# Kernel optimization log

Measured on AMD Instinct MI355X. Metric: run time of the kernel, lower is better.

The kernel has to match this reference:

```python
import jax, jax.numpy as jnp
import numpy as np

N_SEQ = 100_000
N_LAB = 64
E_CON = 1_600_000
D_IN = 128; D_HID = 128; BEL_OUT = 64; INC_OUT = 128
BN_EPS = 1e-5


def setup_inputs() -> dict:
    key = jax.random.key(0)
    ks = jax.random.split(key, 16)
    def W(k, i, o):
        return jax.random.normal(k, (i, o), jnp.float32) / np.float32(np.sqrt(i))
    return {
        "x_seq": jax.random.normal(ks[0], (N_SEQ, D_IN), jnp.float32),
        "x_label": jax.random.normal(ks[1], (N_LAB, D_IN), jnp.float32),
        "W1_bel": W(ks[2], D_IN, D_HID), "b1_bel": jnp.zeros((D_HID,), jnp.float32),
        "W1_inc": W(ks[3], D_IN, D_HID), "b1_inc": jnp.zeros((D_HID,), jnp.float32),
        "W1_con": W(ks[4], D_IN, D_HID), "b1_con": jnp.zeros((D_HID,), jnp.float32),
        "g1s": jnp.ones((D_HID,), jnp.float32), "beta1s": jnp.zeros((D_HID,), jnp.float32),
        "g1l": jnp.ones((D_HID,), jnp.float32), "beta1l": jnp.zeros((D_HID,), jnp.float32),
        "W2_bel": W(ks[5], D_HID, BEL_OUT), "b2_bel": jnp.zeros((BEL_OUT,), jnp.float32),
        "W2_inc": W(ks[6], D_HID, INC_OUT), "b2_inc": jnp.zeros((INC_OUT,), jnp.float32),
        "W2_con": W(ks[7], D_HID, INC_OUT), "b2_con": jnp.zeros((INC_OUT,), jnp.float32),
        "g2s": jnp.ones((INC_OUT,), jnp.float32), "beta2s": jnp.zeros((INC_OUT,), jnp.float32),
        "g2l": jnp.ones((BEL_OUT,), jnp.float32), "beta2l": jnp.zeros((BEL_OUT,), jnp.float32),
        "bel_label": jax.random.randint(ks[8], (N_SEQ,), 0, N_LAB),
        "con_src": jax.random.randint(ks[9], (E_CON,), 0, N_SEQ),
        "con_dst": jax.random.randint(ks[10], (E_CON,), 0, N_SEQ),
    }


def _inv_sqrt_deg(deg):
    # DGL norm='both': deg^{-1/2}, zero-degree nodes get 0
    return jnp.where(deg > 0, jax.lax.rsqrt(jnp.maximum(deg, 1.0)), 0.0)


def _gconv(x_src, src, dst, n_dst, W, b):
    # DGL GraphConv: y = D_dst^{-1/2} A D_src^{-1/2} x W + b
    n_src = x_src.shape[0]
    ones = jnp.ones(src.shape, x_src.dtype)
    deg_out = jax.ops.segment_sum(ones, src, num_segments=n_src)
    deg_in = jax.ops.segment_sum(ones, dst, num_segments=n_dst)
    xs = x_src * _inv_sqrt_deg(deg_out)[:, None]
    agg = jax.ops.segment_sum(xs[src], dst, num_segments=n_dst)  # [n_dst, d]
    agg = agg * _inv_sqrt_deg(deg_in)[:, None]
    return agg @ W + b


def _bn(x, g, b):
    # BatchNorm1d, training mode: biased variance, eps=1e-5
    m = jnp.mean(x, axis=0)
    v = jnp.mean(jnp.square(x - m), axis=0)
    return (x - m) * jax.lax.rsqrt(v + BN_EPS) * g + b


def _hetero_layer(h_seq, h_lab, bel_label, con_src, con_dst, Wb, bb, Wi, bi, Wc, bc):
    seq_idx = jnp.arange(h_seq.shape[0])
    # belongs_to: sequence -> label
    lab = _gconv(h_seq, seq_idx, bel_label, h_lab.shape[0], Wb, bb)
    # including: label -> sequence; connected_to: sequence -> sequence
    inc = _gconv(h_lab, bel_label, seq_idx, h_seq.shape[0], Wi, bi)
    con = _gconv(h_seq, con_src, con_dst, h_seq.shape[0], Wc, bc)
    # HeteroGraphConv aggregate='mean' over relations per dst type
    seq = 0.5 * (inc + con)
    return jax.nn.relu(seq), jax.nn.relu(lab)


def reference(x_seq, x_label,
              W1_bel, b1_bel, W1_inc, b1_inc, W1_con, b1_con,
              g1s, beta1s, g1l, beta1l,
              W2_bel, b2_bel, W2_inc, b2_inc, W2_con, b2_con,
              g2s, beta2s, g2l, beta2l,
              bel_label, con_src, con_dst):
    h_s, h_l = _hetero_layer(x_seq, x_label, bel_label, con_src, con_dst,
                             W1_bel, b1_bel, W1_inc, b1_inc, W1_con, b1_con)
    h_s = _bn(h_s, g1s, beta1s)
    h_l = _bn(h_l, g1l, beta1l)
    h_s, h_l = _hetero_layer(h_s, h_l, bel_label, con_src, con_dst,
                             W2_bel, b2_bel, W2_inc, b2_inc, W2_con, b2_con)
    h_s = _bn(h_s, g2s, beta2s)
    h_l = _bn(h_l, g2l, beta2l)
    return (h_s, h_l)
```

## Files before the change

### kernel.cpp

```cpp
#include <hip/hip_runtime.h>
#include <hip/hip_bf16.h>

#define NSEQ 100000
#define NLAB 64
#define ECON 1600000
#define D 128
#define BN_EPS 1e-5f

#define NB 196
#define BW 512
#define BCAP 10240
#define EPB 4096
#define NPART 32
#define RPB 4096

typedef unsigned int uint32;
typedef unsigned short ushort;
typedef __attribute__((ext_vector_type(8))) short bf16x8;
typedef __attribute__((ext_vector_type(4))) float f32x4;

__device__ __forceinline__ void atomAddF(float* p, float v) {
  unsafeAtomicAdd(p, v);
}
__device__ __forceinline__ float blo(uint32 u) {
  union { uint32 u; float f; } c; c.u = u << 16; return c.f;
}
__device__ __forceinline__ float bhi(uint32 u) {
  union { uint32 u; float f; } c; c.u = u & 0xFFFF0000u; return c.f;
}
__device__ __forceinline__ unsigned short f2b(float f) {
  __hip_bfloat16 h = __float2bfloat16(f);
  union { __hip_bfloat16 h; unsigned short s; } c; c.h = h; return c.s;
}

__global__ __launch_bounds__(256) void k_label_hist(const int* __restrict__ lab, int* cnt) {
  __shared__ int h[NLAB];
  if (threadIdx.x < NLAB) h[threadIdx.x] = 0;
  __syncthreads();
  for (int i = blockIdx.x * 256 + threadIdx.x; i < NSEQ; i += gridDim.x * 256)
    atomicAdd(&h[lab[i]], 1);
  __syncthreads();
  if (threadIdx.x < NLAB) atomicAdd(&cnt[threadIdx.x], h[threadIdx.x]);
}

__global__ __launch_bounds__(256) void k_binA(const int* __restrict__ src,
                                              const int* __restrict__ dst,
                                              int* bucket_cnt, int* sbucket_cnt,
                                              uint32* __restrict__ bpair,
                                              ushort* __restrict__ spair) {
  __shared__ uint32 recD[EPB];
  __shared__ ushort recS[EPB];
  __shared__ unsigned char bidD[EPB];
  __shared__ unsigned char bidS[EPB];
  __shared__ int histD[NB], histS[NB], loffD[NB], loffS[NB], gbD[NB], gbS[NB];
  int t = threadIdx.x;
  for (int i = t; i < NB; i += 256) { histD[i] = 0; histS[i] = 0; }
  __syncthreads();
  int e0 = blockIdx.x * EPB;
  int e1 = min(e0 + EPB, ECON);
  for (int e = e0 + t; e < e1; e += 256) {
    atomicAdd(&histD[dst[e] >> 9], 1);
    atomicAdd(&histS[src[e] >> 9], 1);
  }
  __syncthreads();
  if (t == 0) { int a = 0; for (int i = 0; i < NB; ++i) { loffD[i] = a; a += histD[i]; } }
  if (t == 1) { int a = 0; for (int i = 0; i < NB; ++i) { loffS[i] = a; a += histS[i]; } }
  __syncthreads();
  for (int i = t; i < NB; i += 256) {
    int c = histD[i]; gbD[i] = c ? atomicAdd(&bucket_cnt[i], c) : 0; histD[i] = 0;
    int cs = histS[i]; gbS[i] = cs ? atomicAdd(&sbucket_cnt[i], cs) : 0; histS[i] = 0;
  }
  __syncthreads();
  for (int e = e0 + t; e < e1; e += 256) {
    int s = src[e], d = dst[e];
    int b = d >> 9;
    int p = loffD[b] + atomicAdd(&histD[b], 1);
    recD[p] = (uint32)s | ((uint32)(d & (BW - 1)) << 17);
    bidD[p] = (unsigned char)b;
    int bs = s >> 9;
    int q = loffS[bs] + atomicAdd(&histS[bs], 1);
    recS[q] = (ushort)(s & (BW - 1));
    bidS[q] = (unsigned char)bs;
  }
  __syncthreads();
  int n = e1 - e0;
  for (int i = t; i < n; i += 256) {
    int b = bidD[i];
    bpair[(size_t)b * BCAP + gbD[b] + (i - loffD[b])] = recD[i];
  }
  for (int i = t; i < n; i += 256) {
    int b = bidS[i];
    spair[(size_t)b * BCAP + gbS[b] + (i - loffS[b])] = recS[i];
  }
}

__global__ __launch_bounds__(256) void k_bscan(const int* __restrict__ bucket_cnt,
                                               int* __restrict__ bbase,
                                               const int* __restrict__ cnt_lab,
                                               float* __restrict__ dinv_cnt,
                                               int* __restrict__ lab_base,
                                               int* __restrict__ lab_cursor) {
  int t = threadIdx.x;
  if (t == 0) {
    int acc = 0;
    for (int i = 0; i < NB; ++i) { bbase[i] = acc; acc += bucket_cnt[i]; }
    bbase[NB] = acc;
  }
  if (t == 1) {
    int acc = 0;
    for (int i = 0; i < NLAB; ++i) {
      lab_base[i] = acc; lab_cursor[i] = acc; acc += cnt_lab[i];
    }
    lab_base[NLAB] = acc;
  }
  if (t < NLAB) { int c = cnt_lab[t]; dinv_cnt[t] = c > 0 ? rsqrtf((float)c) : 0.f; }
}

__global__ __launch_bounds__(256) void k_binB(const uint32* __restrict__ bpair,
                                              const int* __restrict__ bucket_cnt,
                                              const int* __restrict__ bbase,
                                              int* __restrict__ off,
                                              float* __restrict__ dinv_in,
                                              int* __restrict__ esrc) {
  __shared__ int deg[BW];
  __shared__ int loff[BW];
  __shared__ int cursor[BW];
  __shared__ int wsum[4];
  int b = blockIdx.x;
  int t = threadIdx.x;
  int cnt = bucket_cnt[b];
  int gbase = bbase[b];
  const uint32* bp = &bpair[(size_t)b * BCAP];
  deg[t] = 0; deg[t + 256] = 0;
  cursor[t] = 0; cursor[t + 256] = 0;
  __syncthreads();
  for (int i = t; i < cnt; i += 256)
    atomicAdd(&deg[bp[i] >> 17], 1);
  __syncthreads();
  int d0 = deg[2 * t], d1 = deg[2 * t + 1];
  int ps = d0 + d1;
  int lane = t & 63, w = t >> 6;
  int v = ps;
  #pragma unroll
  for (int o = 1; o < 64; o <<= 1) { int n = __shfl_up(v, o); if (lane >= o) v += n; }
  if (lane == 63) wsum[w] = v;
  __syncthreads();
  int wbase = 0;
  for (int i = 0; i < w; ++i) wbase += wsum[i];
  int excl = wbase + v - ps;
  loff[2 * t] = excl;
  loff[2 * t + 1] = excl + d0;
  __syncthreads();
  #pragma unroll
  for (int k = 0; k < 2; ++k) {
    int j = t + k * 256;
    int node = b * BW + j;
    if (node < NSEQ) {
      int dg = deg[j];
      off[node] = gbase + loff[j];
      dinv_in[node] = dg > 0 ? rsqrtf((float)dg) : 0.f;
    }
  }
  if (b == NB - 1 && t == 0) off[NSEQ] = ECON;
  for (int i = t; i < cnt; i += 256) {
    uint32 pk = bp[i];
    int dl = pk >> 17;
    int p = gbase + loff[dl] + atomicAdd(&cursor[dl], 1);
    esrc[p] = (int)(pk & 0x1FFFF);
  }
}

__global__ __launch_bounds__(256) void k_binBS(const ushort* __restrict__ spair,
                                               const int* __restrict__ sbucket_cnt,
                                               float* __restrict__ dinv_out) {
  __shared__ int deg[BW];
  int b = blockIdx.x, t = threadIdx.x;
  int cnt = sbucket_cnt[b];
  deg[t] = 0; deg[t + 256] = 0;
  __syncthreads();
  const ushort* sp = &spair[(size_t)b * BCAP];
  for (int i = t; i < cnt; i += 256) atomicAdd(&deg[sp[i]], 1);
  __syncthreads();
  #pragma unroll
  for (int k = 0; k < 2; ++k) {
    int j = t + k * 256;
    int node = b * BW + j;
    if (node < NSEQ) {
      int dg = deg[j];
      dinv_out[node] = dg > 0 ? rsqrtf((float)dg) : 0.f;
    }
  }
}

__global__ __launch_bounds__(256) void k_lab_scatter(const int* __restrict__ lab,
                                                     int* lab_cursor,
                                                     int* __restrict__ lab_sorted) {
  __shared__ int hist[NLAB], base[NLAB];
  int t = threadIdx.x;
  if (t < NLAB) hist[t] = 0;
  __syncthreads();
  int r0 = blockIdx.x * RPB, r1 = min(r0 + RPB, NSEQ);
  for (int r = r0 + t; r < r1; r += 256) atomicAdd(&hist[lab[r]], 1);
  __syncthreads();
  if (t < NLAB) {
    int c = hist[t];
    base[t] = (c > 0) ? atomicAdd(&lab_cursor[t], c) : 0;
    hist[t] = 0;
  }
  __syncthreads();
  for (int r = r0 + t; r < r1; r += 256) {
    int l = lab[r];
    int p = base[l] + atomicAdd(&hist[l], 1);
    lab_sorted[p] = r;
  }
}

__global__ __launch_bounds__(128) void k_bnparams(const float* __restrict__ statsP,
                                                  const float* __restrict__ g,
                                                  const float* __restrict__ beta,
                                                  float* __restrict__ aV,
                                                  float* __restrict__ ccV) {
  int c = threadIdx.x;
  float s = 0.f, q = 0.f;
  #pragma unroll
  for (int k = 0; k < NPART; ++k) {
    s += statsP[k * 256 + c];
    q += statsP[k * 256 + 128 + c];
  }
  const float invN = 1.f / (float)NSEQ;
  float m = s * invN;
  float a = rsqrtf(q * invN - m * m + BN_EPS) * g[c];
  aV[c] = a;
  ccV[c] = beta[c] - m * a;
}

template <int AFFINE>
__global__ __launch_bounds__(256) void k_lab_agg(const uint32* __restrict__ xb,
                                                 const int* __restrict__ lab_sorted,
                                                 const int* __restrict__ lab_base,
                                                 const float* __restrict__ aV,
                                                 const float* __restrict__ ccV,
                                                 float* __restrict__ lab_agg) {
  __shared__ float accs[4][D];
  int t = threadIdx.x;
  int l = blockIdx.x >> 3, p = blockIdx.x & 7;
  int w = t >> 6, cp = t & 63;
  int i0 = lab_base[l], i1 = lab_base[l + 1];
  float ax = 0.f, ay = 0.f;
  for (int i = i0 + p * 4 + w; i < i1; i += 32) {
    int r = lab_sorted[i];
    uint32 u = xb[r * 64 + cp];
    ax += blo(u); ay += bhi(u);
  }
  accs[w][2 * cp] = ax;
  accs[w][2 * cp + 1] = ay;
  __syncthreads();
  if (w == 0) {
    float s0 = accs[0][2 * cp] + accs[1][2 * cp] + accs[2][2 * cp] + accs[3][2 * cp];
    float s1 = accs[0][2 * cp + 1] + accs[1][2 * cp + 1] + accs[2][2 * cp + 1] + accs[3][2 * cp + 1];
    if (AFFINE) {
      s0 *= aV[2 * cp];
      s1 *= aV[2 * cp + 1];
      if (p == 0) {
        float cnt = (float)(i1 - i0);
        s0 += cnt * ccV[2 * cp];
        s1 += cnt * ccV[2 * cp + 1];
      }
    }
    atomAddF(&lab_agg[l * D + 2 * cp], s0);
    atomAddF(&lab_agg[l * D + 2 * cp + 1], s1);
  }
}

__global__ __launch_bounds__(256) void k_cast(const float* __restrict__ x,
                                              uint32* __restrict__ xb) {
  int i = blockIdx.x * 256 + threadIdx.x;
  if (i >= NSEQ * D / 4) return;
  float4 v = ((const float4*)x)[i];
  uint32 u0 = (uint32)f2b(v.x) | ((uint32)f2b(v.y) << 16);
  uint32 u1 = (uint32)f2b(v.z) | ((uint32)f2b(v.w) << 16);
  ((uint2*)xb)[i] = make_uint2(u0, u1);
}

__global__ __launch_bounds__(256) void k_prep_w(const float* __restrict__ W1,
                                                const float* __restrict__ W2,
                                                short* __restrict__ wT1,
                                                short* __restrict__ wT2) {
  int i = blockIdx.x * 256 + threadIdx.x;
  if (i < 16384) {
    int k = i >> 7, c = i & 127;
    wT1[c * 128 + k] = (short)f2b(W1[i]);
  } else if (i < 32768) {
    int j = i - 16384;
    int k = j >> 7, c = j & 127;
    wT2[c * 128 + k] = (short)f2b(W2[j]);
  }
}

__global__ __launch_bounds__(256) void k_mm(
    const float* __restrict__ A, const float* __restrict__ rowscale,
    const float* __restrict__ W, const float* __restrict__ bias,
    float* __restrict__ out, int ncol, int relu) {
  __shared__ float sA[4 * D];
  int tid = threadIdx.x;
  int rows_pb = 256 / ncol;
  int row0 = blockIdx.x * rows_pb;
  int nload = rows_pb * D;
  for (int i = tid; i < nload; i += 256) {
    int r = row0 + (i >> 7);
    float s = rowscale ? rowscale[r] : 1.f;
    sA[i] = A[r * D + (i & 127)] * s;
  }
  __syncthreads();
  int j = tid & (ncol - 1);
  int r = tid / ncol;
  const float* a = &sA[r * D];
  const float* w = &W[j];
  float acc0 = 0.f, acc1 = 0.f, acc2 = 0.f, acc3 = 0.f;
  #pragma unroll 4
  for (int k = 0; k < D; k += 4) {
    acc0 = fmaf(a[k + 0], w[(k + 0) * ncol], acc0);
    acc1 = fmaf(a[k + 1], w[(k + 1) * ncol], acc1);
    acc2 = fmaf(a[k + 2], w[(k + 2) * ncol], acc2);
    acc3 = fmaf(a[k + 3], w[(k + 3) * ncol], acc3);
  }
  float s = (acc0 + acc1) + (acc2 + acc3);
  if (bias) s += bias[j];
  if (relu) s = fmaxf(s, 0.f);
  out[(row0 + r) * ncol + j] = s;
}

__global__ __launch_bounds__(256) void k_label_bn(
    const float* __restrict__ pre,
    const float* __restrict__ g, const float* __restrict__ beta,
    float* __restrict__ out, int ncol) {
  __shared__ float psum[256], psq[256];
  __shared__ float sa[128], sc[128];
  int tid = threadIdx.x;
  int ngrp = 256 / ncol;
  int grp = tid / ncol;
  int col = tid & (ncol - 1);
  float s = 0.f, q = 0.f;
  for (int r = grp; r < NLAB; r += ngrp) {
    float v = pre[r * ncol + col];
    s += v; q += v * v;
  }
  psum[tid] = s; psq[tid] = q;
  __syncthreads();
  if (tid < ncol) {
    float S = 0.f, Q = 0.f;
    for (int gi = 0; gi < ngrp; ++gi) { S += psum[gi * ncol + tid]; Q += psq[gi * ncol + tid]; }
    float m = S * (1.f / NLAB);
    float v = Q * (1.f / NLAB) - m * m;
    float a = rsqrtf(v + BN_EPS) * g[tid];
    sa[tid] = a; sc[tid] = beta[tid] - m * a;
  }
  __syncthreads();
  for (int i = tid; i < NLAB * ncol; i += 256) {
    int c = i & (ncol - 1);
    out[i] = pre[i] * sa[c] + sc[c];
  }
}

template <int AFFINE>
__global__ __launch_bounds__(256) void k_con_agg_bf(
    const uint32* __restrict__ xb, const int* __restrict__ esrc,
    const int* __restrict__ off,
    const float* __restrict__ dinv_out, const float* __restrict__ dinv_in,
    const float* __restrict__ aV, const float* __restrict__ ccV,
    uint32* __restrict__ outb) {
  int wid = (blockIdx.x * 256 + threadIdx.x) >> 6;
  int lane = threadIdx.x & 63;
  if (wid >= NSEQ) return;
  int e0 = off[wid], e1 = off[wid + 1];
  float ax = 0.f, ay = 0.f, sw = 0.f;
  int e = e0;
  for (; e + 3 < e1; e += 4) {
    int s0 = esrc[e], s1 = esrc[e + 1], s2 = esrc[e + 2], s3 = esrc[e + 3];
    float w0 = dinv_out[s0], w1 = dinv_out[s1], w2 = dinv_out[s2], w3 = dinv_out[s3];
    uint32 u0 = xb[s0 * 64 + lane];
    uint32 u1 = xb[s1 * 64 + lane];
    uint32 u2 = xb[s2 * 64 + lane];
    uint32 u3 = xb[s3 * 64 + lane];
    ax += blo(u0) * w0 + blo(u1) * w1 + blo(u2) * w2 + blo(u3) * w3;
    ay += bhi(u0) * w0 + bhi(u1) * w1 + bhi(u2) * w2 + bhi(u3) * w3;
    if (AFFINE) sw += (w0 + w1) + (w2 + w3);
  }
  for (; e < e1; ++e) {
    int s0 = esrc[e];
    float w0 = dinv_out[s0];
    uint32 u0 = xb[s0 * 64 + lane];
    ax += blo(u0) * w0;
    ay += bhi(u0) * w0;
    if (AFFINE) sw += w0;
  }
  float di = dinv_in[wid];
  float rx, ry;
  if (AFFINE) {
    float a0 = aV[2 * lane], a1 = aV[2 * lane + 1];
    float c0 = ccV[2 * lane], c1 = ccV[2 * lane + 1];
    rx = di * fmaf(a0, ax, c0 * sw);
    ry = di * fmaf(a1, ay, c1 * sw);
  } else {
    rx = di * ax;
    ry = di * ay;
  }
  uint32 p = (uint32)f2b(rx) | ((uint32)f2b(ry) << 16);
  outb[wid * 64 + lane] = p;
}

template <int OUTBF>
__global__ __launch_bounds__(256) void k_gemm_mfma(
    const short* __restrict__ aggbf,
    const short* __restrict__ wT,
    const float* __restrict__ b_con,
    const float* __restrict__ y_inc,
    const float* __restrict__ b_inc,
    const float* __restrict__ dinv_cnt,
    const int* __restrict__ bel,
    float* __restrict__ outF,
    short* __restrict__ outB,
    float* __restrict__ statsP) {
  __shared__ short sW[128 * 136];
  __shared__ float csum[D], csq[D];
  int t = threadIdx.x;
  {
    const uint4* src = (const uint4*)wT;
    for (int i = t; i < 2048; i += 256) {
      int row = i >> 4, part = i & 15;
      *(uint4*)&sW[row * 136 + part * 8] = src[i];
    }
  }
  if (t < D) { csum[t] = 0.f; csq[t] = 0.f; }
  int w = t >> 6, l = t & 63;
  int lr = l & 15, lg = l >> 4;
  int row0 = blockIdx.x * 64 + w * 16;
  bf16x8 afrag[4];
  {
    int arow = min(row0 + lr, NSEQ - 1);
    const short* ab = aggbf + arow * 128 + lg * 8;
    #pragma unroll
    for (int kt = 0; kt < 4; ++kt)
      afrag[kt] = *(const bf16x8*)(ab + kt * 32);
  }
  __syncthreads();
  f32x4 acc[8];
  #pragma unroll
  for (int ct = 0; ct < 8; ++ct) {
    f32x4 a = {0.f, 0.f, 0.f, 0.f};
    const short* wb = &sW[(ct * 16 + lr) * 136 + lg * 8];
    #pragma unroll
    for (int kt = 0; kt < 4; ++kt) {
      bf16x8 bfr = *(const bf16x8*)(wb + kt * 32);
      a = __builtin_amdgcn_mfma_f32_16x16x32_bf16(afrag[kt], bfr, a, 0, 0, 0);
    }
    acc[ct] = a;
  }
  int belr[4]; float dcv[4]; int rowv[4];
  #pragma unroll
  for (int r = 0; r < 4; ++r) {
    int gr = row0 + lg * 4 + r;
    rowv[r] = gr;
    int cl = min(gr, NSEQ - 1);
    belr[r] = bel[cl];
    dcv[r] = dinv_cnt[belr[r]];
  }
  #pragma unroll
  for (int ct = 0; ct < 8; ++ct) {
    int col = ct * 16 + lr;
    float bc = b_con[col], bi = b_inc[col];
    float s = 0.f, q = 0.f;
    #pragma unroll
    for (int r = 0; r < 4; ++r) {
      if (rowv[r] < NSEQ) {
        float o = acc[ct][r] + bc + fmaf(dcv[r], y_inc[belr[r] * D + col], bi);
        o = fmaxf(0.5f * o, 0.f);
        if (OUTBF) outB[rowv[r] * D + col] = (short)f2b(o);
        else       outF[rowv[r] * D + col] = o;
        s += o; q += o * o;
      }
    }
    s += __shfl_xor(s, 16); s += __shfl_xor(s, 32);
    q += __shfl_xor(q, 16); q += __shfl_xor(q, 32);
    if (lg == 0) {
      atomicAdd(&csum[col], s);
      atomicAdd(&csq[col], q);
    }
  }
  __syncthreads();
  float* sp = statsP + (blockIdx.x & (NPART - 1)) * 256;
  if (t < D) {
    atomAddF(&sp[t], csum[t]);
    atomAddF(&sp[D + t], csq[t]);
  }
}

__global__ __launch_bounds__(256) void k_bn_apply2(
    float* __restrict__ buf, const float* __restrict__ aV,
    const float* __restrict__ ccV) {
  int t = threadIdx.x;
  int w = t >> 6, cp = t & 63;
  float a0 = aV[2 * cp], a1 = aV[2 * cp + 1];
  float c0 = ccV[2 * cp], c1 = ccV[2 * cp + 1];
  for (int r = blockIdx.x * 4 + w; r < NSEQ; r += gridDim.x * 4) {
    float2 v = ((float2*)buf)[r * 64 + cp];
    v.x = fmaf(v.x, a0, c0);
    v.y = fmaf(v.y, a1, c1);
    ((float2*)buf)[r * 64 + cp] = v;
  }
}

extern "C" void kernel_launch(void* const* d_in, const int* in_sizes, int n_in,
                              void* d_out, int out_size, void* d_ws, size_t ws_size,
                              hipStream_t stream) {
  const float* x_seq   = (const float*)d_in[0];
  const float* x_label = (const float*)d_in[1];
  const float* W1_bel  = (const float*)d_in[2];
  const float* b1_bel  = (const float*)d_in[3];
  const float* W1_inc  = (const float*)d_in[4];
  const float* b1_inc  = (const float*)d_in[5];
  const float* W1_con  = (const float*)d_in[6];
  const float* b1_con  = (const float*)d_in[7];
  const float* g1s     = (const float*)d_in[8];
  const float* beta1s  = (const float*)d_in[9];
  const float* g1l     = (const float*)d_in[10];
  const float* beta1l  = (const float*)d_in[11];
  const float* W2_bel  = (const float*)d_in[12];
  const float* b2_bel  = (const float*)d_in[13];
  const float* W2_inc  = (const float*)d_in[14];
  const float* b2_inc  = (const float*)d_in[15];
  const float* W2_con  = (const float*)d_in[16];
  const float* b2_con  = (const float*)d_in[17];
  const float* g2s     = (const float*)d_in[18];
  const float* beta2s  = (const float*)d_in[19];
  const float* g2l     = (const float*)d_in[20];
  const float* beta2l  = (const float*)d_in[21];
  const int* bel       = (const int*)d_in[22];
  const int* con_src   = (const int*)d_in[23];
  const int* con_dst   = (const int*)d_in[24];
  float* out = (float*)d_out;

  char* ws = (char*)d_ws;
  short*  aggbf    = (short*) (ws);
  short*  h1pre    = (short*) (ws + 25600000);
  uint32* bpair    = (uint32*)(ws + 32000000);
  ushort* spair    = (ushort*)(ws + 40028160);
  int*    esrc     = (int*)   (ws + 51200000);
  float*  dinv_out = (float*) (ws + 57600000);
  int*    cnt_lab     = (int*)  (ws + 58000000);
  int*    bucket_cnt  = (int*)  (ws + 58001024);
  int*    sbucket_cnt = (int*)  (ws + 58002048);
  float*  statsP1     = (float*)(ws + 58003072);
  float*  statsP2     = (float*)(ws + 58035840);
  float*  lab_agg1    = (float*)(ws + 58068608);
  float*  lab_agg2    = (float*)(ws + 58101376);
  float*  dinv_in    = (float*)(ws + 58134144);
  float*  dinv_cnt   = (float*)(ws + 58534144);
  int*    bbase      = (int*)  (ws + 58534400);
  int*    off        = (int*)  (ws + 58535424);
  float*  y_inc1     = (float*)(ws + 58935552);
  float*  y_inc2     = (float*)(ws + 58968320);
  float*  h_l1       = (float*)(ws + 59001088);
  short*  wT1        = (short*)(ws + 59033856);
  short*  wT2        = (short*)(ws + 59066624);
  int*    lab_base   = (int*)  (ws + 59099392);
  int*    lab_cursor = (int*)  (ws + 59100416);
  int*    lab_sorted = (int*)  (ws + 59101440);
  float*  ab1        = (float*)(ws + 59501440);
  float*  cc1        = (float*)(ws + 59501952);
  float*  ab2        = (float*)(ws + 59502464);
  float*  cc2        = (float*)(ws + 59502976);

  uint32* xb = (uint32*)out;
  float* belp1 = (float*)ws;
  float* belp2 = (float*)ws;

  hipMemsetAsync(ws + 58000000, 0, 134144, stream);

  k_label_hist <<<256, 256, 0, stream>>>(bel, cnt_lab);
  k_binA       <<<(ECON + EPB - 1) / EPB, 256, 0, stream>>>(con_src, con_dst,
                                                            bucket_cnt, sbucket_cnt,
                                                            bpair, spair);
  k_bscan      <<<1, 256, 0, stream>>>(bucket_cnt, bbase, cnt_lab, dinv_cnt,
                                       lab_base, lab_cursor);
  k_binB       <<<NB, 256, 0, stream>>>(bpair, bucket_cnt, bbase,
                                        off, dinv_in, esrc);
  k_binBS      <<<NB, 256, 0, stream>>>(spair, sbucket_cnt, dinv_out);
  k_lab_scatter<<<(NSEQ + RPB - 1) / RPB, 256, 0, stream>>>(bel, lab_cursor, lab_sorted);
  k_cast       <<<(NSEQ * D / 4 + 255) / 256, 256, 0, stream>>>(x_seq, xb);
  k_prep_w     <<<128, 256, 0, stream>>>(W1_con, W2_con, wT1, wT2);

  k_lab_agg<0> <<<NLAB * 8, 256, 0, stream>>>(xb, lab_sorted, lab_base,
                                              nullptr, nullptr, lab_agg1);
  k_mm         <<<32, 256, 0, stream>>>(x_label, nullptr, W1_inc, nullptr, y_inc1, 128, 0);
  k_mm         <<<32, 256, 0, stream>>>(lab_agg1, dinv_cnt, W1_bel, b1_bel, belp1, 128, 1);
  k_label_bn   <<<1, 256, 0, stream>>>(belp1, g1l, beta1l, h_l1, 128);
  k_con_agg_bf<0><<<NSEQ / 4, 256, 0, stream>>>(xb, esrc, off, dinv_out, dinv_in,
                                                nullptr, nullptr, (uint32*)aggbf);
  k_gemm_mfma<1><<<(NSEQ + 63) / 64, 256, 0, stream>>>(
                   aggbf, wT1, b1_con, y_inc1, b1_inc, dinv_cnt, bel,
                   nullptr, h1pre, statsP1);
  k_bnparams   <<<1, 128, 0, stream>>>(statsP1, g1s, beta1s, ab1, cc1);

  k_lab_agg<1> <<<NLAB * 8, 256, 0, stream>>>((const uint32*)h1pre, lab_sorted,
                                              lab_base, ab1, cc1, lab_agg2);
  k_mm         <<<32, 256, 0, stream>>>(h_l1, nullptr, W2_inc, nullptr, y_inc2, 128, 0);
  k_mm         <<<16, 256, 0, stream>>>(lab_agg2, dinv_cnt, W2_bel, b2_bel, belp2, 64, 1);
  k_label_bn   <<<1, 256, 0, stream>>>(belp2, g2l, beta2l, out + (size_t)NSEQ * D, 64);
  k_con_agg_bf<1><<<NSEQ / 4, 256, 0, stream>>>((const uint32*)h1pre, esrc, off,
                                                dinv_out, dinv_in, ab1, cc1,
                                                (uint32*)aggbf);
  k_gemm_mfma<0><<<(NSEQ + 63) / 64, 256, 0, stream>>>(
                   aggbf, wT2, b2_con, y_inc2, b2_inc, dinv_cnt, bel,
                   out, nullptr, statsP2);
  k_bnparams   <<<1, 128, 0, stream>>>(statsP2, g2s, beta2s, ab2, cc2);
  k_bn_apply2  <<<1024, 256, 0, stream>>>(out, ab2, cc2);
}
```

Measured before the change: 433.6 us.

## Split connected-edge aggregation into column slices for cache locality

The CSR gather for the sequence-to-sequence relation now gives each block a 256-row chunk and one of 8 column slices (16 features). Eight lanes cover a row's slice, and 32 row groups walk the chunk. The idea is that blocks working on the same slice touch only a 1/8-wide band of the bf16 feature matrix, so the random source-row gathers reuse L2 lines better. The cost is that esrc, off and dinv_out are now read 8 times, and each gather fetches only 32 bytes per row, which may waste sector bandwidth.

```diff
diff --git a/kernel.cpp b/kernel.cpp
--- a/kernel.cpp
+++ b/kernel.cpp
@@ -363,50 +363,54 @@
 }
 
 template <int AFFINE>
-__global__ __launch_bounds__(256) void k_con_agg_bf(
+__global__ __launch_bounds__(256) void k_con_agg_sl(
     const uint32* __restrict__ xb, const int* __restrict__ esrc,
     const int* __restrict__ off,
     const float* __restrict__ dinv_out, const float* __restrict__ dinv_in,
     const float* __restrict__ aV, const float* __restrict__ ccV,
     uint32* __restrict__ outb) {
-  int wid = (blockIdx.x * 256 + threadIdx.x) >> 6;
-  int lane = threadIdx.x & 63;
-  if (wid >= NSEQ) return;
-  int e0 = off[wid], e1 = off[wid + 1];
-  float ax = 0.f, ay = 0.f, sw = 0.f;
-  int e = e0;
-  for (; e + 3 < e1; e += 4) {
-    int s0 = esrc[e], s1 = esrc[e + 1], s2 = esrc[e + 2], s3 = esrc[e + 3];
-    float w0 = dinv_out[s0], w1 = dinv_out[s1], w2 = dinv_out[s2], w3 = dinv_out[s3];
-    uint32 u0 = xb[s0 * 64 + lane];
-    uint32 u1 = xb[s1 * 64 + lane];
-    uint32 u2 = xb[s2 * 64 + lane];
-    uint32 u3 = xb[s3 * 64 + lane];
-    ax += blo(u0) * w0 + blo(u1) * w1 + blo(u2) * w2 + blo(u3) * w3;
-    ay += bhi(u0) * w0 + bhi(u1) * w1 + bhi(u2) * w2 + bhi(u3) * w3;
-    if (AFFINE) sw += (w0 + w1) + (w2 + w3);
-  }
-  for (; e < e1; ++e) {
-    int s0 = esrc[e];
-    float w0 = dinv_out[s0];
-    uint32 u0 = xb[s0 * 64 + lane];
-    ax += blo(u0) * w0;
-    ay += bhi(u0) * w0;
-    if (AFFINE) sw += w0;
-  }
-  float di = dinv_in[wid];
-  float rx, ry;
+  int slice = blockIdx.x & 7;
+  int chunk = blockIdx.x >> 3;
+  int g = threadIdx.x >> 3;
+  int j = threadIdx.x & 7;
+  int colu = slice * 8 + j;
+  float a0 = 0.f, a1 = 0.f, c0 = 0.f, c1 = 0.f;
   if (AFFINE) {
-    float a0 = aV[2 * lane], a1 = aV[2 * lane + 1];
-    float c0 = ccV[2 * lane], c1 = ccV[2 * lane + 1];
-    rx = di * fmaf(a0, ax, c0 * sw);
-    ry = di * fmaf(a1, ay, c1 * sw);
-  } else {
-    rx = di * ax;
-    ry = di * ay;
-  }
-  uint32 p = (uint32)f2b(rx) | ((uint32)f2b(ry) << 16);
-  outb[wid * 64 + lane] = p;
+    a0 = aV[2 * colu]; a1 = aV[2 * colu + 1];
+    c0 = ccV[2 * colu]; c1 = ccV[2 * colu + 1];
+  }
+  int rowEnd = min(chunk * 256 + 256, NSEQ);
+  for (int row = chunk * 256 + g; row < rowEnd; row += 32) {
+    int e = off[row], e1 = off[row + 1];
+    float ax = 0.f, ay = 0.f, sw = 0.f;
+    for (; e + 1 < e1; e += 2) {
+      int s0 = esrc[e], s1 = esrc[e + 1];
+      float w0 = dinv_out[s0], w1 = dinv_out[s1];
+      uint32 u0 = xb[s0 * 64 + colu];
+      uint32 u1 = xb[s1 * 64 + colu];
+      ax += blo(u0) * w0 + blo(u1) * w1;
+      ay += bhi(u0) * w0 + bhi(u1) * w1;
+      if (AFFINE) sw += w0 + w1;
+    }
+    if (e < e1) {
+      int s0 = esrc[e];
+      float w0 = dinv_out[s0];
+      uint32 u0 = xb[s0 * 64 + colu];
+      ax += blo(u0) * w0;
+      ay += bhi(u0) * w0;
+      if (AFFINE) sw += w0;
+    }
+    float di = dinv_in[row];
+    float rx, ry;
+    if (AFFINE) {
+      rx = di * fmaf(a0, ax, c0 * sw);
+      ry = di * fmaf(a1, ay, c1 * sw);
+    } else {
+      rx = di * ax;
+      ry = di * ay;
+    }
+    outb[row * 64 + colu] = (uint32)f2b(rx) | ((uint32)f2b(ry) << 16);
+  }
 }
 
 template <int OUTBF>
@@ -590,12 +594,14 @@
   k_cast       <<<(NSEQ * D / 4 + 255) / 256, 256, 0, stream>>>(x_seq, xb);
   k_prep_w     <<<128, 256, 0, stream>>>(W1_con, W2_con, wT1, wT2);
 
+  const int CON_GRID = 8 * ((NSEQ + 255) / 256);
+
   k_lab_agg<0> <<<NLAB * 8, 256, 0, stream>>>(xb, lab_sorted, lab_base,
                                               nullptr, nullptr, lab_agg1);
   k_mm         <<<32, 256, 0, stream>>>(x_label, nullptr, W1_inc, nullptr, y_inc1, 128, 0);
   k_mm         <<<32, 256, 0, stream>>>(lab_agg1, dinv_cnt, W1_bel, b1_bel, belp1, 128, 1);
   k_label_bn   <<<1, 256, 0, stream>>>(belp1, g1l, beta1l, h_l1, 128);
-  k_con_agg_bf<0><<<NSEQ / 4, 256, 0, stream>>>(xb, esrc, off, dinv_out, dinv_in,
+  k_con_agg_sl<0><<<CON_GRID, 256, 0, stream>>>(xb, esrc, off, dinv_out, dinv_in,
                                                 nullptr, nullptr, (uint32*)aggbf);
   k_gemm_mfma<1><<<(NSEQ + 63) / 64, 256, 0, stream>>>(
                    aggbf, wT1, b1_con, y_inc1, b1_inc, dinv_cnt, bel,
@@ -607,7 +613,7 @@
   k_mm         <<<32, 256, 0, stream>>>(h_l1, nullptr, W2_inc, nullptr, y_inc2, 128, 0);
   k_mm         <<<16, 256, 0, stream>>>(lab_agg2, dinv_cnt, W2_bel, b2_bel, belp2, 64, 1);
   k_label_bn   <<<1, 256, 0, stream>>>(belp2, g2l, beta2l, out + (size_t)NSEQ * D, 64);
-  k_con_agg_bf<1><<<NSEQ / 4, 256, 0, stream>>>((const uint32*)h1pre, esrc, off,
+  k_con_agg_sl<1><<<CON_GRID, 256, 0, stream>>>((const uint32*)h1pre, esrc, off,
                                                 dinv_out, dinv_in, ab1, cc1,
                                                 (uint32*)aggbf);
   k_gemm_mfma<0><<<(NSEQ + 63) / 64, 256, 0, stream>>>(
```

After: 723.6 us. 1.67x slower.
